# Kernel optimization log

Hardware: AMD Instinct MI355X
Metric: run time of the kernel (lower is better)

Reference implementation:

```python
import jax, jax.numpy as jnp
import numpy as np

N = 100000   # nodes
E = 1600000  # edges per relation
R = 4        # relations
D = 128      # feature dim (in == hidden == out)


def setup_inputs() -> dict:
    key = jax.random.key(0)
    ks = jax.random.split(key, 8)
    x = jax.random.normal(ks[0], (N, D), jnp.float32)
    src = jax.random.randint(ks[1], (R, E), 0, N)
    dst = jax.random.randint(ks[2], (R, E), 0, N)
    ew = jax.random.uniform(ks[3], (R, E), jnp.float32)
    W1 = jax.random.normal(ks[4], (R, D, D), jnp.float32) / np.float32(np.sqrt(D))
    b1 = jax.random.normal(ks[5], (R, D), jnp.float32) * 0.02
    W2 = jax.random.normal(ks[6], (R, D, D), jnp.float32) / np.float32(np.sqrt(D))
    b2 = jax.random.normal(ks[7], (R, D), jnp.float32) * 0.02
    return {"x": x, "src": src, "dst": dst, "ew": ew,
            "W1": W1, "b1": b1, "W2": W2, "b2": b2}


def _graph_conv(h, W, b, src_r, dst_r, ew_r):
    # DGL GraphConv, norm='both': unweighted degrees clamped to >=1.
    ones = jnp.ones(src_r.shape[0], h.dtype)
    deg_out = jnp.clip(jax.ops.segment_sum(ones, src_r, num_segments=N), 1.0)
    deg_in = jnp.clip(jax.ops.segment_sum(ones, dst_r, num_segments=N), 1.0)
    hs = h * jax.lax.rsqrt(deg_out)[:, None]
    hs = hs @ W                                   # [N, D] dense transform
    m = hs[src_r] * ew_r[:, None]                 # gather + edge weight [E, D]
    agg = jax.ops.segment_sum(m, dst_r, num_segments=N)  # scatter-add [N, D]
    return agg * jax.lax.rsqrt(deg_in)[:, None] + b


def reference(x, src, dst, ew, W1, b1, W2, b2):
    def hetero_layer(h, W, b):
        out = _graph_conv(h, W[0], b[0], src[0], dst[0], ew[0])
        for r in range(1, R):  # sum-aggregate over relations
            out = out + _graph_conv(h, W[r], b[r], src[r], dst[r], ew[r])
        return jax.nn.relu(out)  # HeteroRelu

    h = hetero_layer(x, W1, b1)
    return hetero_layer(h, W2, b2)
```

## Files before the change

### kernel.cpp

```cpp
#include <hip/hip_runtime.h>
#include <hip/hip_bf16.h>
#include <cstdint>
#include <cstddef>

#define N_NODE 100000
#define N_EDGE 1600000
#define N_REL  4
#define DIM    128
#define KDIM   512
#define HALF_N 50000
#define CHUNK  2048
#define NCH    ((N_NODE + CHUNK - 1) / CHUNK)

#define CH_E   50000
#define NCHUNK 32
#define TS     25000
#define NTILE  4

typedef __attribute__((ext_vector_type(8))) short bf16x8;
typedef __attribute__((ext_vector_type(4))) float f32x4;

__device__ inline unsigned short f2bf(float f) {
    __hip_bfloat16 b = __float2bfloat16(f);
    return *reinterpret_cast<unsigned short*>(&b);
}

__global__ __launch_bounds__(512) void k_hist(const int* __restrict__ idx,
                                              int* __restrict__ P) {
    __shared__ unsigned hist[TS / 2];
    int c = blockIdx.x, t = blockIdx.y, r = blockIdx.z;
    for (int i = threadIdx.x; i < TS / 2; i += 512) hist[i] = 0;
    __syncthreads();
    int n0 = t * TS;
    const int4* ip = (const int4*)(idx + (size_t)r * N_EDGE + c * CH_E);
    for (int q = threadIdx.x * 2; q < CH_E / 4; q += 1024) {
        int4 d0 = ip[q], d1 = ip[q + 1];
        int dd[8] = {d0.x, d0.y, d0.z, d0.w, d1.x, d1.y, d1.z, d1.w};
#pragma unroll
        for (int i = 0; i < 8; ++i) {
            unsigned a = (unsigned)(dd[i] - n0);
            if (a < TS) atomicAdd(&hist[a >> 1], 1u << (16 * (a & 1)));
        }
    }
    __syncthreads();
    int* Pp = P + ((size_t)r * NCHUNK + c) * N_NODE;
    for (int i = threadIdx.x; i < TS; i += 512) {
        int n = n0 + i;
        if (n < N_NODE)
            Pp[n] = (int)((hist[i >> 1] >> (16 * (i & 1))) & 0xffffu);
    }
}

__global__ void k_reduce_rinv(const int* __restrict__ Pd, const int* __restrict__ Ps,
                              int* __restrict__ cnt_in, float* __restrict__ rinv_in,
                              float* __restrict__ rinv_out) {
    int i = blockIdx.x * blockDim.x + threadIdx.x;
    if (i >= N_REL * N_NODE) return;
    int r = i / N_NODE, n = i - r * N_NODE;
    int ci = 0, co = 0;
#pragma unroll
    for (int c = 0; c < NCHUNK; ++c) {
        ci += Pd[((size_t)r * NCHUNK + c) * N_NODE + n];
        co += Ps[((size_t)r * NCHUNK + c) * N_NODE + n];
    }
    cnt_in[i]   = ci;
    rinv_in[i]  = rsqrtf((float)max(ci, 1));
    rinv_out[i] = rsqrtf((float)max(co, 1));
}

__global__ void k_chunk_sum(const int* __restrict__ cnt_in, int* __restrict__ partials) {
    int r = blockIdx.y, ch = blockIdx.x;
    __shared__ int sdata[256];
    int s = 0;
    for (int i = 0; i < CHUNK / 256; ++i) {
        int n = ch * CHUNK + i * 256 + threadIdx.x;
        if (n < N_NODE) s += cnt_in[r * N_NODE + n];
    }
    sdata[threadIdx.x] = s;
    __syncthreads();
    for (int off = 128; off > 0; off >>= 1) {
        if (threadIdx.x < off) sdata[threadIdx.x] += sdata[threadIdx.x + off];
        __syncthreads();
    }
    if (threadIdx.x == 0) partials[r * NCH + ch] = sdata[0];
}

__global__ void k_scan_partials(const int* __restrict__ partials,
                                int* __restrict__ chunk_base, int* __restrict__ row_ptr) {
    __shared__ int sp[N_REL * NCH];
    int t = threadIdx.x;
    if (t < N_REL * NCH) sp[t] = partials[t];
    __syncthreads();
    if (t == 0) {
        for (int r = 0; r < N_REL; ++r) {
            int run = 0;
            for (int ch = 0; ch < NCH; ++ch) {
                chunk_base[r * NCH + ch] = run;
                run += sp[r * NCH + ch];
            }
            row_ptr[r * (N_NODE + 1) + N_NODE] = N_EDGE;
        }
    }
}

__global__ void k_chunk_scan(const int* __restrict__ cnt_in,
                             const int* __restrict__ chunk_base, int* __restrict__ row_ptr) {
    int r = blockIdx.y, ch = blockIdx.x;
    __shared__ int tsum[256];
    int base_n = ch * CHUNK;
    int vals[8];
    int loc = 0;
    for (int i = 0; i < 8; ++i) {
        int n = base_n + threadIdx.x * 8 + i;
        vals[i] = (n < N_NODE) ? cnt_in[r * N_NODE + n] : 0;
        loc += vals[i];
    }
    tsum[threadIdx.x] = loc;
    __syncthreads();
    for (int off = 1; off < 256; off <<= 1) {
        int y = (threadIdx.x >= off) ? tsum[threadIdx.x - off] : 0;
        __syncthreads();
        tsum[threadIdx.x] += y;
        __syncthreads();
    }
    int pos = chunk_base[r * NCH + ch] + tsum[threadIdx.x] - loc;
    for (int i = 0; i < 8; ++i) {
        int n = base_n + threadIdx.x * 8 + i;
        if (n < N_NODE) { row_ptr[r * (N_NODE + 1) + n] = pos; pos += vals[i]; }
    }
}

__global__ void k_base(int* __restrict__ P, const int* __restrict__ row_ptr) {
    int i = blockIdx.x * blockDim.x + threadIdx.x;
    if (i >= N_REL * N_NODE) return;
    int r = i / N_NODE, n = i - r * N_NODE;
    int run = row_ptr[r * (N_NODE + 1) + n];
#pragma unroll
    for (int c = 0; c < NCHUNK; ++c) {
        size_t o = ((size_t)r * NCHUNK + c) * N_NODE + n;
        int p = P[o];
        P[o] = run;
        run += p;
    }
}

__global__ __launch_bounds__(512) void k_scatter5(const int* __restrict__ src,
                          const int* __restrict__ dst, const float* __restrict__ ew,
                          const int* __restrict__ base, const float* __restrict__ rinv_out,
                          int2* __restrict__ pk_s) {
    __shared__ unsigned cur[TS / 2];
    int c = blockIdx.x, t = blockIdx.y, r = blockIdx.z;
    for (int i = threadIdx.x; i < TS / 2; i += 512) cur[i] = 0;
    __syncthreads();
    int n0 = t * TS;
    int e0 = c * CH_E;
    const int*   bp = base + ((size_t)r * NCHUNK + c) * N_NODE + n0;
    const float* ro = rinv_out + (size_t)r * N_NODE;
    size_t roff = (size_t)r * N_EDGE;
    for (int e = e0 + threadIdx.x * 4; e < e0 + CH_E; e += 2048) {
        int4   d4 = *(const int4*)  (dst + roff + e);
        int4   s4 = *(const int4*)  (src + roff + e);
        float4 w4 = *(const float4*)(ew  + roff + e);
        unsigned a; unsigned old; int rank;
        a = (unsigned)(d4.x - n0);
        if (a < TS) {
            old = atomicAdd(&cur[a >> 1], 1u << (16 * (a & 1)));
            rank = (int)((old >> (16 * (a & 1))) & 0xffffu);
            pk_s[roff + bp[a] + rank] = make_int2(s4.x, __float_as_int(w4.x * ro[s4.x]));
        }
        a = (unsigned)(d4.y - n0);
        if (a < TS) {
            old = atomicAdd(&cur[a >> 1], 1u << (16 * (a & 1)));
            rank = (int)((old >> (16 * (a & 1))) & 0xffffu);
            pk_s[roff + bp[a] + rank] = make_int2(s4.y, __float_as_int(w4.y * ro[s4.y]));
        }
        a = (unsigned)(d4.z - n0);
        if (a < TS) {
            old = atomicAdd(&cur[a >> 1], 1u << (16 * (a & 1)));
            rank = (int)((old >> (16 * (a & 1))) & 0xffffu);
            pk_s[roff + bp[a] + rank] = make_int2(s4.z, __float_as_int(w4.z * ro[s4.z]));
        }
        a = (unsigned)(d4.w - n0);
        if (a < TS) {
            old = atomicAdd(&cur[a >> 1], 1u << (16 * (a & 1)));
            rank = (int)((old >> (16 * (a & 1))) & 0xffffu);
            pk_s[roff + bp[a] + rank] = make_int2(s4.w, __float_as_int(w4.w * ro[s4.w]));
        }
    }
}

__global__ void k_cvt(const float* __restrict__ x, unsigned short* __restrict__ xb) {
    int i = blockIdx.x * blockDim.x + threadIdx.x;
    if (i >= N_NODE * DIM / 4) return;
    float4 v = ((const float4*)x)[i];
    ushort4 o;
    o.x = f2bf(v.x); o.y = f2bf(v.y); o.z = f2bf(v.z); o.w = f2bf(v.w);
    ((ushort4*)xb)[i] = o;
}

__global__ void k_cvt_w(const float* __restrict__ W, unsigned short* __restrict__ WT) {
    int i = blockIdx.x * blockDim.x + threadIdx.x;
    if (i >= KDIM * DIM) return;
    int k = i >> 7, j = i & 127;
    WT[(size_t)j * KDIM + k] = f2bf(W[i]);
}

#define FMA8(u, cc) do { \
    acc0 += (cc) * __uint_as_float((unsigned)(u).x << 16); \
    acc1 += (cc) * __uint_as_float((unsigned)(u).x & 0xffff0000u); \
    acc2 += (cc) * __uint_as_float((unsigned)(u).y << 16); \
    acc3 += (cc) * __uint_as_float((unsigned)(u).y & 0xffff0000u); \
    acc4 += (cc) * __uint_as_float((unsigned)(u).z << 16); \
    acc5 += (cc) * __uint_as_float((unsigned)(u).z & 0xffff0000u); \
    acc6 += (cc) * __uint_as_float((unsigned)(u).w << 16); \
    acc7 += (cc) * __uint_as_float((unsigned)(u).w & 0xffff0000u); } while (0)

__global__ __launch_bounds__(256) void k_spmm4(const int* __restrict__ row_ptr,
                        const int2* __restrict__ pk_s,
                        const float* __restrict__ rinv_in, const int4* __restrict__ hb4,
                        int4* __restrict__ Tb4, int node0) {
    int wv   = threadIdx.x >> 6;
    int lane = threadIdx.x & 63;
    int r    = lane >> 4;
    int m    = lane & 15;
    int nl   = blockIdx.x * 4 + wv;
    int node = node0 + nl;
    int k0 = row_ptr[r * (N_NODE + 1) + node];
    int k1 = row_ptr[r * (N_NODE + 1) + node + 1];
    const int2* pp = pk_s + (size_t)r * N_EDGE;
    float acc0 = 0.f, acc1 = 0.f, acc2 = 0.f, acc3 = 0.f;
    float acc4 = 0.f, acc5 = 0.f, acc6 = 0.f, acc7 = 0.f;
    int k = k0;
    for (; k + 7 < k1; k += 8) {
        int2 p0 = pp[k],     p1 = pp[k + 1], p2 = pp[k + 2], p3 = pp[k + 3];
        int2 p4 = pp[k + 4], p5 = pp[k + 5], p6 = pp[k + 6], p7 = pp[k + 7];
        int4 u0 = hb4[(size_t)p0.x * 16 + m];
        int4 u1 = hb4[(size_t)p1.x * 16 + m];
        int4 u2 = hb4[(size_t)p2.x * 16 + m];
        int4 u3 = hb4[(size_t)p3.x * 16 + m];
        int4 u4 = hb4[(size_t)p4.x * 16 + m];
        int4 u5 = hb4[(size_t)p5.x * 16 + m];
        int4 u6 = hb4[(size_t)p6.x * 16 + m];
        int4 u7 = hb4[(size_t)p7.x * 16 + m];
        FMA8(u0, __int_as_float(p0.y));
        FMA8(u1, __int_as_float(p1.y));
        FMA8(u2, __int_as_float(p2.y));
        FMA8(u3, __int_as_float(p3.y));
        FMA8(u4, __int_as_float(p4.y));
        FMA8(u5, __int_as_float(p5.y));
        FMA8(u6, __int_as_float(p6.y));
        FMA8(u7, __int_as_float(p7.y));
    }
    if (k + 3 < k1) {
        int2 p0 = pp[k], p1 = pp[k + 1], p2 = pp[k + 2], p3 = pp[k + 3];
        int4 u0 = hb4[(size_t)p0.x * 16 + m];
        int4 u1 = hb4[(size_t)p1.x * 16 + m];
        int4 u2 = hb4[(size_t)p2.x * 16 + m];
        int4 u3 = hb4[(size_t)p3.x * 16 + m];
        FMA8(u0, __int_as_float(p0.y));
        FMA8(u1, __int_as_float(p1.y));
        FMA8(u2, __int_as_float(p2.y));
        FMA8(u3, __int_as_float(p3.y));
        k += 4;
    }
    if (k + 1 < k1) {
        int2 p0 = pp[k], p1 = pp[k + 1];
        int4 u0 = hb4[(size_t)p0.x * 16 + m];
        int4 u1 = hb4[(size_t)p1.x * 16 + m];
        FMA8(u0, __int_as_float(p0.y));
        FMA8(u1, __int_as_float(p1.y));
        k += 2;
    }
    if (k < k1) {
        int2 p0 = pp[k];
        int4 u0 = hb4[(size_t)p0.x * 16 + m];
        FMA8(u0, __int_as_float(p0.y));
    }
    float ri = rinv_in[r * N_NODE + node];
    int4 o;
    o.x = (int)(((unsigned)f2bf(acc1 * ri) << 16) | (unsigned)f2bf(acc0 * ri));
    o.y = (int)(((unsigned)f2bf(acc3 * ri) << 16) | (unsigned)f2bf(acc2 * ri));
    o.z = (int)(((unsigned)f2bf(acc5 * ri) << 16) | (unsigned)f2bf(acc4 * ri));
    o.w = (int)(((unsigned)f2bf(acc7 * ri) << 16) | (unsigned)f2bf(acc6 * ri));
    Tb4[(size_t)nl * 64 + r * 16 + m] = o;
}

__global__ __launch_bounds__(256) void k_gemm(const unsigned short* __restrict__ Tb,
                                              const unsigned short* __restrict__ WT,
                                              const float* __restrict__ b,
                                              float* __restrict__ outf,
                                              unsigned short* __restrict__ outb,
                                              int node0) {
    int lane = threadIdx.x & 63;
    int wv   = threadIdx.x >> 6;
    int row0 = blockIdx.x * 64 + wv * 16;
    if (row0 >= HALF_N) return;
    int m  = lane & 15;
    int kg = lane >> 4;

    f32x4 acc[8];
#pragma unroll
    for (int t = 0; t < 8; ++t) acc[t] = (f32x4){0.f, 0.f, 0.f, 0.f};

    const unsigned short* arow = Tb + (size_t)(row0 + m) * KDIM + kg * 8;
    for (int k0 = 0; k0 < KDIM; k0 += 32) {
        bf16x8 af = *(const bf16x8*)(arow + k0);
#pragma unroll
        for (int t = 0; t < 8; ++t) {
            bf16x8 bf = *(const bf16x8*)(WT + (size_t)(t * 16 + m) * KDIM + k0 + kg * 8);
            acc[t] = __builtin_amdgcn_mfma_f32_16x16x32_bf16(af, bf, acc[t], 0, 0, 0);
        }
    }

    int rbase = row0 + kg * 4;
#pragma unroll
    for (int t = 0; t < 8; ++t) {
        int col = t * 16 + m;
        float bs = b[col] + b[DIM + col] + b[2 * DIM + col] + b[3 * DIM + col];
#pragma unroll
        for (int rg = 0; rg < 4; ++rg) {
            float v = acc[t][rg] + bs;
            v = v > 0.f ? v : 0.f;
            size_t o = (size_t)(node0 + rbase + rg) * DIM + col;
            if (outb) outb[o] = f2bf(v);
            else      outf[o] = v;
        }
    }
}

extern "C" void kernel_launch(void* const* d_in, const int* in_sizes, int n_in,
                              void* d_out, int out_size, void* d_ws, size_t ws_size,
                              hipStream_t stream) {
    const float* x   = (const float*)d_in[0];
    const int*   src = (const int*)  d_in[1];
    const int*   dst = (const int*)  d_in[2];
    const float* ew  = (const float*)d_in[3];
    const float* W1  = (const float*)d_in[4];
    const float* b1  = (const float*)d_in[5];
    const float* W2  = (const float*)d_in[6];
    const float* b2  = (const float*)d_in[7];
    float* out = (float*)d_out;

    char* p = (char*)d_ws;
    auto alloc = [&](size_t bytes) -> char* {
        char* q = p;
        p += (bytes + 255) & ~(size_t)255;
        return q;
    };
    const size_t RN = (size_t)N_REL * N_NODE;
    int*   cnt_in     = (int*)  alloc(RN * 4);
    float* rinv_out   = (float*)alloc(RN * 4);
    float* rinv_in    = (float*)alloc(RN * 4);
    int*   row_ptr    = (int*)  alloc((size_t)N_REL * (N_NODE + 1) * 4);
    int*   partials   = (int*)  alloc(N_REL * NCH * 4);
    int*   chunk_base = (int*)  alloc(N_REL * NCH * 4);
    unsigned short* WT1b = (unsigned short*)alloc((size_t)KDIM * DIM * 2);
    unsigned short* WT2b = (unsigned short*)alloc((size_t)KDIM * DIM * 2);
    int2*  pk_s       = (int2*) alloc((size_t)N_REL * N_EDGE * 8);
    char*  Treg       =         alloc((size_t)HALF_N * KDIM * 2);
    char*  hreg       =         alloc((size_t)N_REL * NCHUNK * N_NODE * 4);

    int* Pd = (int*)Treg;
    int* Ps = (int*)hreg;
    unsigned short* h_mid_b = (unsigned short*)hreg;
    unsigned short* xb      = (unsigned short*)(hreg + (size_t)N_NODE * DIM * 2);
    unsigned short* Tb      = (unsigned short*)Treg;

    dim3 gridH(NCHUNK, NTILE, N_REL);
    k_hist<<<gridH, 512, 0, stream>>>(dst, Pd);
    k_hist<<<gridH, 512, 0, stream>>>(src, Ps);
    k_reduce_rinv<<<((int)RN + 255) / 256, 256, 0, stream>>>(Pd, Ps, cnt_in, rinv_in, rinv_out);
    k_cvt<<<(N_NODE * DIM / 4 + 255) / 256, 256, 0, stream>>>(x, xb);
    k_cvt_w<<<(KDIM * DIM + 255) / 256, 256, 0, stream>>>(W1, WT1b);
    k_cvt_w<<<(KDIM * DIM + 255) / 256, 256, 0, stream>>>(W2, WT2b);
    k_chunk_sum<<<dim3(NCH, N_REL), 256, 0, stream>>>(cnt_in, partials);
    k_scan_partials<<<1, 256, 0, stream>>>(partials, chunk_base, row_ptr);
    k_chunk_scan<<<dim3(NCH, N_REL), 256, 0, stream>>>(cnt_in, chunk_base, row_ptr);
    k_base<<<((int)RN + 255) / 256, 256, 0, stream>>>(Pd, row_ptr);
    k_scatter5<<<gridH, 512, 0, stream>>>(src, dst, ew, Pd, rinv_out, pk_s);

    const int spmm_grid = HALF_N / 4;
    const int gemm_grid = (HALF_N + 63) / 64;

    for (int h = 0; h < 2; ++h) {
        k_spmm4<<<spmm_grid, 256, 0, stream>>>(row_ptr, pk_s, rinv_in,
                                               (const int4*)xb, (int4*)Tb, h * HALF_N);
        k_gemm<<<gemm_grid, 256, 0, stream>>>(Tb, WT1b, b1, (float*)nullptr, h_mid_b, h * HALF_N);
    }
    for (int h = 0; h < 2; ++h) {
        k_spmm4<<<spmm_grid, 256, 0, stream>>>(row_ptr, pk_s, rinv_in,
                                               (const int4*)h_mid_b, (int4*)Tb, h * HALF_N);
        k_gemm<<<gemm_grid, 256, 0, stream>>>(Tb, WT2b, b2, out, (unsigned short*)nullptr, h * HALF_N);
    }
}
```

Measured before the change: 1.222 ms.

## Fuse SpMM aggregation and dense GEMM into one kernel via LDS staging

The separate gather-aggregate and MFMA GEMM kernels, run over two node halves, are merged into one kernel per layer. Each block aggregates 64 nodes across all four relations into an XOR-swizzled 64 KB LDS tile, then runs the bf16 MFMA GEMM from LDS with bias and ReLU. This removes the global write and read of the intermediate [N,512] bf16 buffer and cuts kernel launches. In exchange, the large LDS footprint limits resident blocks per CU, which may reduce latency hiding for the irregular gathers, and the GEMM cannot start until a block's gathers finish.

```diff
diff --git a/kernel.cpp b/kernel.cpp
--- a/kernel.cpp
+++ b/kernel.cpp
@@ -8,7 +8,6 @@
 #define N_REL  4
 #define DIM    128
 #define KDIM   512
-#define HALF_N 50000
 #define CHUNK  2048
 #define NCH    ((N_NODE + CHUNK - 1) / CHUNK)
 
@@ -215,115 +214,130 @@
     acc6 += (cc) * __uint_as_float((unsigned)(u).w << 16); \
     acc7 += (cc) * __uint_as_float((unsigned)(u).w & 0xffff0000u); } while (0)
 
-__global__ __launch_bounds__(256) void k_spmm4(const int* __restrict__ row_ptr,
+__global__ __launch_bounds__(512, 4) void k_fused(const int* __restrict__ row_ptr,
                         const int2* __restrict__ pk_s,
                         const float* __restrict__ rinv_in, const int4* __restrict__ hb4,
-                        int4* __restrict__ Tb4, int node0) {
+                        const unsigned short* __restrict__ WT,
+                        const float* __restrict__ b,
+                        float* __restrict__ outf, unsigned short* __restrict__ outb) {
+    __shared__ unsigned short Als[64 * KDIM];
+    int node_base = blockIdx.x * 64;
+    int limit = N_NODE - node_base;
+    int lane = threadIdx.x & 63;
+    int m = lane & 15;
+
+    {
+        int g = threadIdx.x >> 4;
+        for (int i = 0; i < 8; ++i) {
+            int tt = g + 32 * i;
+            int nl = tt >> 2, r = tt & 3;
+            unsigned lds_off = (unsigned)nl * (KDIM * 2)
+                             + (((unsigned)(r * 256 + m * 16)) ^ (((unsigned)nl & 7u) << 4));
+            if (nl >= limit) {
+                *(int4*)((char*)Als + lds_off) = make_int4(0, 0, 0, 0);
+                continue;
+            }
+            int node = node_base + nl;
+            int k0 = row_ptr[r * (N_NODE + 1) + node];
+            int k1 = row_ptr[r * (N_NODE + 1) + node + 1];
+            const int2* pp = pk_s + (size_t)r * N_EDGE;
+            float acc0 = 0.f, acc1 = 0.f, acc2 = 0.f, acc3 = 0.f;
+            float acc4 = 0.f, acc5 = 0.f, acc6 = 0.f, acc7 = 0.f;
+            int k = k0;
+            for (; k + 7 < k1; k += 8) {
+                int2 p0 = pp[k],     p1 = pp[k + 1], p2 = pp[k + 2], p3 = pp[k + 3];
+                int2 p4 = pp[k + 4], p5 = pp[k + 5], p6 = pp[k + 6], p7 = pp[k + 7];
+                int4 u0 = hb4[(size_t)p0.x * 16 + m];
+                int4 u1 = hb4[(size_t)p1.x * 16 + m];
+                int4 u2 = hb4[(size_t)p2.x * 16 + m];
+                int4 u3 = hb4[(size_t)p3.x * 16 + m];
+                int4 u4 = hb4[(size_t)p4.x * 16 + m];
+                int4 u5 = hb4[(size_t)p5.x * 16 + m];
+                int4 u6 = hb4[(size_t)p6.x * 16 + m];
+                int4 u7 = hb4[(size_t)p7.x * 16 + m];
+                FMA8(u0, __int_as_float(p0.y));
+                FMA8(u1, __int_as_float(p1.y));
+                FMA8(u2, __int_as_float(p2.y));
+                FMA8(u3, __int_as_float(p3.y));
+                FMA8(u4, __int_as_float(p4.y));
+                FMA8(u5, __int_as_float(p5.y));
+                FMA8(u6, __int_as_float(p6.y));
+                FMA8(u7, __int_as_float(p7.y));
+            }
+            if (k + 3 < k1) {
+                int2 p0 = pp[k], p1 = pp[k + 1], p2 = pp[k + 2], p3 = pp[k + 3];
+                int4 u0 = hb4[(size_t)p0.x * 16 + m];
+                int4 u1 = hb4[(size_t)p1.x * 16 + m];
+                int4 u2 = hb4[(size_t)p2.x * 16 + m];
+                int4 u3 = hb4[(size_t)p3.x * 16 + m];
+                FMA8(u0, __int_as_float(p0.y));
+                FMA8(u1, __int_as_float(p1.y));
+                FMA8(u2, __int_as_float(p2.y));
+                FMA8(u3, __int_as_float(p3.y));
+                k += 4;
+            }
+            if (k + 1 < k1) {
+                int2 p0 = pp[k], p1 = pp[k + 1];
+                int4 u0 = hb4[(size_t)p0.x * 16 + m];
+                int4 u1 = hb4[(size_t)p1.x * 16 + m];
+                FMA8(u0, __int_as_float(p0.y));
+                FMA8(u1, __int_as_float(p1.y));
+                k += 2;
+            }
+            if (k < k1) {
+                int2 p0 = pp[k];
+                int4 u0 = hb4[(size_t)p0.x * 16 + m];
+                FMA8(u0, __int_as_float(p0.y));
+            }
+            float ri = rinv_in[r * N_NODE + node];
+            int4 o;
+            o.x = (int)(((unsigned)f2bf(acc1 * ri) << 16) | (unsigned)f2bf(acc0 * ri));
+            o.y = (int)(((unsigned)f2bf(acc3 * ri) << 16) | (unsigned)f2bf(acc2 * ri));
+            o.z = (int)(((unsigned)f2bf(acc5 * ri) << 16) | (unsigned)f2bf(acc4 * ri));
+            o.w = (int)(((unsigned)f2bf(acc7 * ri) << 16) | (unsigned)f2bf(acc6 * ri));
+            *(int4*)((char*)Als + lds_off) = o;
+        }
+    }
+    __syncthreads();
+
     int wv   = threadIdx.x >> 6;
-    int lane = threadIdx.x & 63;
-    int r    = lane >> 4;
-    int m    = lane & 15;
-    int nl   = blockIdx.x * 4 + wv;
-    int node = node0 + nl;
-    int k0 = row_ptr[r * (N_NODE + 1) + node];
-    int k1 = row_ptr[r * (N_NODE + 1) + node + 1];
-    const int2* pp = pk_s + (size_t)r * N_EDGE;
-    float acc0 = 0.f, acc1 = 0.f, acc2 = 0.f, acc3 = 0.f;
-    float acc4 = 0.f, acc5 = 0.f, acc6 = 0.f, acc7 = 0.f;
-    int k = k0;
-    for (; k + 7 < k1; k += 8) {
-        int2 p0 = pp[k],     p1 = pp[k + 1], p2 = pp[k + 2], p3 = pp[k + 3];
-        int2 p4 = pp[k + 4], p5 = pp[k + 5], p6 = pp[k + 6], p7 = pp[k + 7];
-        int4 u0 = hb4[(size_t)p0.x * 16 + m];
-        int4 u1 = hb4[(size_t)p1.x * 16 + m];
-        int4 u2 = hb4[(size_t)p2.x * 16 + m];
-        int4 u3 = hb4[(size_t)p3.x * 16 + m];
-        int4 u4 = hb4[(size_t)p4.x * 16 + m];
-        int4 u5 = hb4[(size_t)p5.x * 16 + m];
-        int4 u6 = hb4[(size_t)p6.x * 16 + m];
-        int4 u7 = hb4[(size_t)p7.x * 16 + m];
-        FMA8(u0, __int_as_float(p0.y));
-        FMA8(u1, __int_as_float(p1.y));
-        FMA8(u2, __int_as_float(p2.y));
-        FMA8(u3, __int_as_float(p3.y));
-        FMA8(u4, __int_as_float(p4.y));
-        FMA8(u5, __int_as_float(p5.y));
-        FMA8(u6, __int_as_float(p6.y));
-        FMA8(u7, __int_as_float(p7.y));
-    }
-    if (k + 3 < k1) {
-        int2 p0 = pp[k], p1 = pp[k + 1], p2 = pp[k + 2], p3 = pp[k + 3];
-        int4 u0 = hb4[(size_t)p0.x * 16 + m];
-        int4 u1 = hb4[(size_t)p1.x * 16 + m];
-        int4 u2 = hb4[(size_t)p2.x * 16 + m];
-        int4 u3 = hb4[(size_t)p3.x * 16 + m];
-        FMA8(u0, __int_as_float(p0.y));
-        FMA8(u1, __int_as_float(p1.y));
-        FMA8(u2, __int_as_float(p2.y));
-        FMA8(u3, __int_as_float(p3.y));
-        k += 4;
-    }
-    if (k + 1 < k1) {
-        int2 p0 = pp[k], p1 = pp[k + 1];
-        int4 u0 = hb4[(size_t)p0.x * 16 + m];
-        int4 u1 = hb4[(size_t)p1.x * 16 + m];
-        FMA8(u0, __int_as_float(p0.y));
-        FMA8(u1, __int_as_float(p1.y));
-        k += 2;
-    }
-    if (k < k1) {
-        int2 p0 = pp[k];
-        int4 u0 = hb4[(size_t)p0.x * 16 + m];
-        FMA8(u0, __int_as_float(p0.y));
-    }
-    float ri = rinv_in[r * N_NODE + node];
-    int4 o;
-    o.x = (int)(((unsigned)f2bf(acc1 * ri) << 16) | (unsigned)f2bf(acc0 * ri));
-    o.y = (int)(((unsigned)f2bf(acc3 * ri) << 16) | (unsigned)f2bf(acc2 * ri));
-    o.z = (int)(((unsigned)f2bf(acc5 * ri) << 16) | (unsigned)f2bf(acc4 * ri));
-    o.w = (int)(((unsigned)f2bf(acc7 * ri) << 16) | (unsigned)f2bf(acc6 * ri));
-    Tb4[(size_t)nl * 64 + r * 16 + m] = o;
-}
-
-__global__ __launch_bounds__(256) void k_gemm(const unsigned short* __restrict__ Tb,
-                                              const unsigned short* __restrict__ WT,
-                                              const float* __restrict__ b,
-                                              float* __restrict__ outf,
-                                              unsigned short* __restrict__ outb,
-                                              int node0) {
-    int lane = threadIdx.x & 63;
-    int wv   = threadIdx.x >> 6;
-    int row0 = blockIdx.x * 64 + wv * 16;
-    if (row0 >= HALF_N) return;
-    int m  = lane & 15;
-    int kg = lane >> 4;
-
-    f32x4 acc[8];
-#pragma unroll
-    for (int t = 0; t < 8; ++t) acc[t] = (f32x4){0.f, 0.f, 0.f, 0.f};
-
-    const unsigned short* arow = Tb + (size_t)(row0 + m) * KDIM + kg * 8;
+    int row0 = (wv >> 1) * 16;
+    int col0 = (wv & 1) * 64;
+    int kg   = lane >> 4;
+
+    f32x4 acc[4];
+#pragma unroll
+    for (int t = 0; t < 4; ++t) acc[t] = (f32x4){0.f, 0.f, 0.f, 0.f};
+
+    int arow = row0 + m;
+    unsigned abase = (unsigned)arow * (KDIM * 2);
+    unsigned axor  = ((unsigned)arow & 7u) << 4;
     for (int k0 = 0; k0 < KDIM; k0 += 32) {
-        bf16x8 af = *(const bf16x8*)(arow + k0);
-#pragma unroll
-        for (int t = 0; t < 8; ++t) {
-            bf16x8 bf = *(const bf16x8*)(WT + (size_t)(t * 16 + m) * KDIM + k0 + kg * 8);
+        unsigned aoff = abase + ((((unsigned)(k0 + kg * 8)) * 2u) ^ axor);
+        bf16x8 af = *(const bf16x8*)((const char*)Als + aoff);
+#pragma unroll
+        for (int t = 0; t < 4; ++t) {
+            int col = col0 + t * 16 + m;
+            bf16x8 bf = *(const bf16x8*)(WT + (size_t)col * KDIM + k0 + kg * 8);
             acc[t] = __builtin_amdgcn_mfma_f32_16x16x32_bf16(af, bf, acc[t], 0, 0, 0);
         }
     }
 
-    int rbase = row0 + kg * 4;
-#pragma unroll
-    for (int t = 0; t < 8; ++t) {
-        int col = t * 16 + m;
+#pragma unroll
+    for (int t = 0; t < 4; ++t) {
+        int col = col0 + t * 16 + m;
         float bs = b[col] + b[DIM + col] + b[2 * DIM + col] + b[3 * DIM + col];
 #pragma unroll
         for (int rg = 0; rg < 4; ++rg) {
-            float v = acc[t][rg] + bs;
-            v = v > 0.f ? v : 0.f;
-            size_t o = (size_t)(node0 + rbase + rg) * DIM + col;
-            if (outb) outb[o] = f2bf(v);
-            else      outf[o] = v;
+            int row = row0 + kg * 4 + rg;
+            int node = node_base + row;
+            if (node < N_NODE) {
+                float v = acc[t][rg] + bs;
+                v = v > 0.f ? v : 0.f;
+                size_t o = (size_t)node * DIM + col;
+                if (outb) outb[o] = f2bf(v);
+                else      outf[o] = v;
+            }
         }
     }
 }
@@ -357,14 +371,13 @@
     unsigned short* WT1b = (unsigned short*)alloc((size_t)KDIM * DIM * 2);
     unsigned short* WT2b = (unsigned short*)alloc((size_t)KDIM * DIM * 2);
     int2*  pk_s       = (int2*) alloc((size_t)N_REL * N_EDGE * 8);
-    char*  Treg       =         alloc((size_t)HALF_N * KDIM * 2);
+    char*  Treg       =         alloc((size_t)N_REL * NCHUNK * N_NODE * 4);
     char*  hreg       =         alloc((size_t)N_REL * NCHUNK * N_NODE * 4);
 
     int* Pd = (int*)Treg;
     int* Ps = (int*)hreg;
     unsigned short* h_mid_b = (unsigned short*)hreg;
     unsigned short* xb      = (unsigned short*)(hreg + (size_t)N_NODE * DIM * 2);
-    unsigned short* Tb      = (unsigned short*)Treg;
 
     dim3 gridH(NCHUNK, NTILE, N_REL);
     k_hist<<<gridH, 512, 0, stream>>>(dst, Pd);
@@ -379,17 +392,12 @@
     k_base<<<((int)RN + 255) / 256, 256, 0, stream>>>(Pd, row_ptr);
     k_scatter5<<<gridH, 512, 0, stream>>>(src, dst, ew, Pd, rinv_out, pk_s);
 
-    const int spmm_grid = HALF_N / 4;
-    const int gemm_grid = (HALF_N + 63) / 64;
-
-    for (int h = 0; h < 2; ++h) {
-        k_spmm4<<<spmm_grid, 256, 0, stream>>>(row_ptr, pk_s, rinv_in,
-                                               (const int4*)xb, (int4*)Tb, h * HALF_N);
-        k_gemm<<<gemm_grid, 256, 0, stream>>>(Tb, WT1b, b1, (float*)nullptr, h_mid_b, h * HALF_N);
-    }
-    for (int h = 0; h < 2; ++h) {
-        k_spmm4<<<spmm_grid, 256, 0, stream>>>(row_ptr, pk_s, rinv_in,
-                                               (const int4*)h_mid_b, (int4*)Tb, h * HALF_N);
-        k_gemm<<<gemm_grid, 256, 0, stream>>>(Tb, WT2b, b2, out, (unsigned short*)nullptr, h * HALF_N);
-    }
-}
+    const int fused_grid = (N_NODE + 63) / 64;
+
+    k_fused<<<fused_grid, 512, 0, stream>>>(row_ptr, pk_s, rinv_in,
+                                            (const int4*)xb, WT1b, b1,
+                                            (float*)nullptr, h_mid_b);
+    k_fused<<<fused_grid, 512, 0, stream>>>(row_ptr, pk_s, rinv_in,
+                                            (const int4*)h_mid_b, WT2b, b2,
+                                            out, (unsigned short*)nullptr);
+}
```

Measured after the change: 1.136 ms. 1.08x faster.
